# Kernel optimization log

Measured on AMD Instinct MI355X. Metric: run time of the kernel, lower is better.

## Reference

```python
import jax, jax.numpy as jnp
import numpy as np

S = 16          # spatial_size (adaptive pool output per dim)
EPS = 1e-8      # torch.cosine_similarity eps

def _avg_pool3d(x, s):
    # exact adaptive avg pool when D,H,W divisible by s
    B, C, D, H, W = x.shape
    kd, kh, kw = D // s, H // s, W // s
    x = x.reshape(B, C, s, kd, s, kh, s, kw)
    return x.mean(axis=(3, 5, 7))  # (B, C, s, s, s)

def _flatten_rows(x):
    # (B,C,s,s,s) -> (B*s^3, C), matching view+transpose+flatten
    B, C = x.shape[0], x.shape[1]
    return x.reshape(B, C, -1).transpose(0, 2, 1).reshape(-1, C)

def _cos_sim_matrix(a):
    # pairwise cosine similarity via normalize + GEMM
    norms = jnp.maximum(jnp.linalg.norm(a, axis=-1, keepdims=True), EPS)
    an = a / norms
    return an @ an.T  # (N, N)

def setup_inputs() -> dict:
    key = jax.random.key(0)
    k1, k2 = jax.random.split(key)
    shape = (2, 32, 64, 64, 64)
    p1 = jax.random.normal(k1, shape, dtype=jnp.float32)
    p2 = jax.random.normal(k2, shape, dtype=jnp.float32)
    return {"p1": p1, "p2": p2}

def reference(p1, p2):
    aa = _flatten_rows(_avg_pool3d(p1, S))  # (N, C), N = B*S^3
    bb = _flatten_rows(_avg_pool3d(p2, S))
    sim_a = _cos_sim_matrix(aa)
    sim_b = _cos_sim_matrix(bb)
    return jnp.mean((sim_a - sim_b) ** 2)  # MSELoss
```

## Files before the change

kernel.cpp:

```cpp
#include <hip/hip_runtime.h>
#include <hip/hip_bf16.h>


#define HW    4096
#define DHW   262144
#define NROW  8192
#define C     32
#define NPART 8

__global__ __launch_bounds__(1024) void pool_norm_kernel(
    const float* __restrict__ p1, const float* __restrict__ p2,
    float* __restrict__ An, float* __restrict__ Bn)
{
    const int bid = blockIdx.x;
    const int yo = bid & 15;
    const int zo = (bid >> 4) & 15;
    const int b  = bid >> 8;

    const float* __restrict__ src = (blockIdx.y == 0) ? p1 : p2;
    float* __restrict__ dst       = (blockIdx.y == 0) ? An : Bn;

    const int tid  = threadIdx.x;
    const int wv   = tid >> 6;
    const int lane = tid & 63;
    const int dy   = lane >> 4;
    const int x4   = lane & 15;

    __shared__ float pool[C][16];
    __shared__ float inv_norm[16];

    float4 v[2][4];
    #pragma unroll
    for (int cc = 0; cc < 2; ++cc) {
        const int c = wv * 2 + cc;
        const float* base = src + (size_t)(b * C + c) * DHW
                          + (4 * zo) * HW + (4 * yo + dy) * 64 + 4 * x4;
        #pragma unroll
        for (int dz = 0; dz < 4; ++dz)
            v[cc][dz] = *reinterpret_cast<const float4*>(base + dz * HW);
    }

    #pragma unroll
    for (int cc = 0; cc < 2; ++cc) {
        float s = 0.f;
        #pragma unroll
        for (int dz = 0; dz < 4; ++dz)
            s += (v[cc][dz].x + v[cc][dz].y) + (v[cc][dz].z + v[cc][dz].w);
        s += __shfl_xor(s, 16);
        s += __shfl_xor(s, 32);
        if (lane < 16) pool[wv * 2 + cc][lane] = s * (1.0f / 64.0f);
    }
    __syncthreads();

    if (tid < 16) {
        float ss = 0.f;
        #pragma unroll
        for (int c = 0; c < C; ++c) { const float p = pool[c][tid]; ss += p * p; }
        inv_norm[tid] = 1.0f / fmaxf(sqrtf(ss), 1e-8f);
    }
    __syncthreads();

    if (tid < 512) {
        const int x = tid >> 5;
        const int c = tid & 31;
        const int row = ((b * 16 + zo) * 16 + yo) * 16 + x;
        dst[(size_t)row * C + c] = pool[c][x] * inv_norm[x];
    }
}

__global__ __launch_bounds__(256) void gram_kernel(
    const float* __restrict__ An, const float* __restrict__ Bn,
    float* __restrict__ G)
{
    const int tid = threadIdx.x;
    const int k  = tid >> 3;
    const int l4 = (tid & 7) * 4;

    __shared__ float As[32 * C];
    __shared__ float Bs[32 * C];

    float gaa[4] = {0.f, 0.f, 0.f, 0.f};
    float gab[4] = {0.f, 0.f, 0.f, 0.f};
    float gbb[4] = {0.f, 0.f, 0.f, 0.f};

    const int r = blockIdx.x * 32;
    reinterpret_cast<float4*>(As)[tid] =
        reinterpret_cast<const float4*>(An + (size_t)r * C)[tid];
    reinterpret_cast<float4*>(Bs)[tid] =
        reinterpret_cast<const float4*>(Bn + (size_t)r * C)[tid];
    __syncthreads();

    #pragma unroll
    for (int i = 0; i < 32; ++i) {
        const float a_k = As[i * C + k];
        const float b_k = Bs[i * C + k];
        const float4 a_l = *reinterpret_cast<const float4*>(&As[i * C + l4]);
        const float4 b_l = *reinterpret_cast<const float4*>(&Bs[i * C + l4]);
        gaa[0] += a_k * a_l.x;  gaa[1] += a_k * a_l.y;
        gaa[2] += a_k * a_l.z;  gaa[3] += a_k * a_l.w;
        gab[0] += a_k * b_l.x;  gab[1] += a_k * b_l.y;
        gab[2] += a_k * b_l.z;  gab[3] += a_k * b_l.w;
        gbb[0] += b_k * b_l.x;  gbb[1] += b_k * b_l.y;
        gbb[2] += b_k * b_l.z;  gbb[3] += b_k * b_l.w;
    }

    float* Gp = G + (size_t)(blockIdx.x & (NPART - 1)) * 3072;
    #pragma unroll
    for (int j = 0; j < 4; ++j) {
        atomicAdd(&Gp[k * C + l4 + j],        gaa[j]);
        atomicAdd(&Gp[1024 + k * C + l4 + j], gab[j]);
        atomicAdd(&Gp[2048 + k * C + l4 + j], gbb[j]);
    }
}

__global__ __launch_bounds__(1024) void finalize_kernel(
    const float* __restrict__ G, float* __restrict__ out)
{
    const int t = threadIdx.x;
    float gaa = 0.f, gab = 0.f, gbb = 0.f;
    #pragma unroll
    for (int p = 0; p < NPART; ++p) {
        gaa += G[p * 3072 + t];
        gab += G[p * 3072 + 1024 + t];
        gbb += G[p * 3072 + 2048 + t];
    }
    float v = gaa * gaa + gbb * gbb - 2.f * gab * gab;

    __shared__ float red[16];
    #pragma unroll
    for (int off = 32; off > 0; off >>= 1) v += __shfl_down(v, off);
    if ((t & 63) == 0) red[t >> 6] = v;
    __syncthreads();
    if (t < 16) {
        float w = red[t];
        #pragma unroll
        for (int off = 8; off > 0; off >>= 1) w += __shfl_down(w, off);
        if (t == 0) out[0] = w / ((float)NROW * (float)NROW);
    }
}

extern "C" void kernel_launch(void* const* d_in, const int* in_sizes, int n_in,
                              void* d_out, int out_size, void* d_ws, size_t ws_size,
                              hipStream_t stream) {
    const float* p1 = (const float*)d_in[0];
    const float* p2 = (const float*)d_in[1];
    float* out = (float*)d_out;

    float* An = (float*)d_ws;
    float* Bn = An + (size_t)NROW * C;
    float* G  = Bn + (size_t)NROW * C;

    hipMemsetAsync(G, 0, NPART * 3072 * sizeof(float), stream);

    dim3 g1(512, 2);
    pool_norm_kernel<<<g1, 1024, 0, stream>>>(p1, p2, An, Bn);
    gram_kernel<<<256, 256, 0, stream>>>(An, Bn, G);
    finalize_kernel<<<1, 1024, 0, stream>>>(G, out);
}
```

Before: 160.7 us.

## Fuse pooling, normalization and Gram accumulation into one kernel

Merges the pool+normalize kernel and the Gram-matrix kernel into a single kernel. Each block loads both p1 and p2 tiles, pools and normalizes in shared memory, then computes its 32x32 partial Gram products directly and atomically adds them to 16 partition buffers. This removes the intermediate An/Bn round trip through global memory and one kernel launch. In exchange it halves the grid, doubles per-thread loads and registers, and raises atomic traffic, since 512 blocks now add 3072 values each.

```diff
diff --git a/kernel.cpp b/kernel.cpp
--- a/kernel.cpp
+++ b/kernel.cpp
@@ -6,19 +6,16 @@
 #define DHW   262144
 #define NROW  8192
 #define C     32
-#define NPART 8
+#define NPART 16
 
-__global__ __launch_bounds__(1024) void pool_norm_kernel(
+__global__ __launch_bounds__(1024) void fused_pool_gram_kernel(
     const float* __restrict__ p1, const float* __restrict__ p2,
-    float* __restrict__ An, float* __restrict__ Bn)
+    float* __restrict__ G)
 {
     const int bid = blockIdx.x;
     const int yo = bid & 15;
     const int zo = (bid >> 4) & 15;
     const int b  = bid >> 8;
-
-    const float* __restrict__ src = (blockIdx.y == 0) ? p1 : p2;
-    float* __restrict__ dst       = (blockIdx.y == 0) ? An : Bn;
 
     const int tid  = threadIdx.x;
     const int wv   = tid >> 6;
@@ -26,91 +23,86 @@
     const int dy   = lane >> 4;
     const int x4   = lane & 15;
 
-    __shared__ float pool[C][16];
-    __shared__ float inv_norm[16];
+    __shared__ float pa[C][17];
+    __shared__ float pb[C][17];
+    __shared__ float inva[16];
+    __shared__ float invb[16];
 
-    float4 v[2][4];
+    const size_t sp_off = (size_t)(4 * zo) * HW + (size_t)(4 * yo + dy) * 64 + 4 * x4;
+
+    float4 va[2][4], vb[2][4];
     #pragma unroll
     for (int cc = 0; cc < 2; ++cc) {
         const int c = wv * 2 + cc;
-        const float* base = src + (size_t)(b * C + c) * DHW
-                          + (4 * zo) * HW + (4 * yo + dy) * 64 + 4 * x4;
+        const float* basea = p1 + (size_t)(b * C + c) * DHW + sp_off;
+        const float* baseb = p2 + (size_t)(b * C + c) * DHW + sp_off;
         #pragma unroll
-        for (int dz = 0; dz < 4; ++dz)
-            v[cc][dz] = *reinterpret_cast<const float4*>(base + dz * HW);
+        for (int dz = 0; dz < 4; ++dz) {
+            va[cc][dz] = *reinterpret_cast<const float4*>(basea + dz * HW);
+            vb[cc][dz] = *reinterpret_cast<const float4*>(baseb + dz * HW);
+        }
     }
+    __builtin_amdgcn_sched_barrier(0);
 
     #pragma unroll
     for (int cc = 0; cc < 2; ++cc) {
-        float s = 0.f;
+        float sa = 0.f, sb = 0.f;
         #pragma unroll
-        for (int dz = 0; dz < 4; ++dz)
-            s += (v[cc][dz].x + v[cc][dz].y) + (v[cc][dz].z + v[cc][dz].w);
-        s += __shfl_xor(s, 16);
-        s += __shfl_xor(s, 32);
-        if (lane < 16) pool[wv * 2 + cc][lane] = s * (1.0f / 64.0f);
+        for (int dz = 0; dz < 4; ++dz) {
+            sa += (va[cc][dz].x + va[cc][dz].y) + (va[cc][dz].z + va[cc][dz].w);
+            sb += (vb[cc][dz].x + vb[cc][dz].y) + (vb[cc][dz].z + vb[cc][dz].w);
+        }
+        sa += __shfl_xor(sa, 16);  sa += __shfl_xor(sa, 32);
+        sb += __shfl_xor(sb, 16);  sb += __shfl_xor(sb, 32);
+        if (lane < 16) {
+            pa[wv * 2 + cc][lane] = sa * (1.0f / 64.0f);
+            pb[wv * 2 + cc][lane] = sb * (1.0f / 64.0f);
+        }
     }
     __syncthreads();
 
-    if (tid < 16) {
+    if (tid < 32) {
+        const int x = tid & 15;
         float ss = 0.f;
-        #pragma unroll
-        for (int c = 0; c < C; ++c) { const float p = pool[c][tid]; ss += p * p; }
-        inv_norm[tid] = 1.0f / fmaxf(sqrtf(ss), 1e-8f);
+        if (tid < 16) {
+            #pragma unroll
+            for (int c2 = 0; c2 < C; ++c2) { const float v = pa[c2][x]; ss += v * v; }
+            inva[x] = 1.0f / fmaxf(sqrtf(ss), 1e-8f);
+        } else {
+            #pragma unroll
+            for (int c2 = 0; c2 < C; ++c2) { const float v = pb[c2][x]; ss += v * v; }
+            invb[x] = 1.0f / fmaxf(sqrtf(ss), 1e-8f);
+        }
     }
     __syncthreads();
 
-    if (tid < 512) {
-        const int x = tid >> 5;
-        const int c = tid & 31;
-        const int row = ((b * 16 + zo) * 16 + yo) * 16 + x;
-        dst[(size_t)row * C + c] = pool[c][x] * inv_norm[x];
+    {
+        const int sel = tid >> 9;
+        const int c   = (tid >> 4) & 31;
+        const int x   = tid & 15;
+        if (sel == 0) pa[c][x] *= inva[x];
+        else          pb[c][x] *= invb[x];
     }
-}
-
-__global__ __launch_bounds__(256) void gram_kernel(
-    const float* __restrict__ An, const float* __restrict__ Bn,
-    float* __restrict__ G)
-{
-    const int tid = threadIdx.x;
-    const int k  = tid >> 3;
-    const int l4 = (tid & 7) * 4;
-
-    __shared__ float As[32 * C];
-    __shared__ float Bs[32 * C];
-
-    float gaa[4] = {0.f, 0.f, 0.f, 0.f};
-    float gab[4] = {0.f, 0.f, 0.f, 0.f};
-    float gbb[4] = {0.f, 0.f, 0.f, 0.f};
-
-    const int r = blockIdx.x * 32;
-    reinterpret_cast<float4*>(As)[tid] =
-        reinterpret_cast<const float4*>(An + (size_t)r * C)[tid];
-    reinterpret_cast<float4*>(Bs)[tid] =
-        reinterpret_cast<const float4*>(Bn + (size_t)r * C)[tid];
     __syncthreads();
 
+    const int k = tid >> 5;
+    const int l = tid & 31;
+    float gaa = 0.f, gab = 0.f, gbb = 0.f;
     #pragma unroll
-    for (int i = 0; i < 32; ++i) {
-        const float a_k = As[i * C + k];
-        const float b_k = Bs[i * C + k];
-        const float4 a_l = *reinterpret_cast<const float4*>(&As[i * C + l4]);
-        const float4 b_l = *reinterpret_cast<const float4*>(&Bs[i * C + l4]);
-        gaa[0] += a_k * a_l.x;  gaa[1] += a_k * a_l.y;
-        gaa[2] += a_k * a_l.z;  gaa[3] += a_k * a_l.w;
-        gab[0] += a_k * b_l.x;  gab[1] += a_k * b_l.y;
-        gab[2] += a_k * b_l.z;  gab[3] += a_k * b_l.w;
-        gbb[0] += b_k * b_l.x;  gbb[1] += b_k * b_l.y;
-        gbb[2] += b_k * b_l.z;  gbb[3] += b_k * b_l.w;
+    for (int x = 0; x < 16; ++x) {
+        const float ak = pa[k][x];
+        const float al = pa[l][x];
+        const float bk = pb[k][x];
+        const float bl = pb[l][x];
+        gaa += ak * al;
+        gab += ak * bl;
+        gbb += bk * bl;
     }
 
-    float* Gp = G + (size_t)(blockIdx.x & (NPART - 1)) * 3072;
-    #pragma unroll
-    for (int j = 0; j < 4; ++j) {
-        atomicAdd(&Gp[k * C + l4 + j],        gaa[j]);
-        atomicAdd(&Gp[1024 + k * C + l4 + j], gab[j]);
-        atomicAdd(&Gp[2048 + k * C + l4 + j], gbb[j]);
-    }
+    float* Gp = G + (size_t)(bid & (NPART - 1)) * 3072;
+    atomicAdd(&Gp[       k * 32 + l], gaa);
+    atomicAdd(&Gp[1024 + k * 32 + l], gab);
+    atomicAdd(&Gp[2048 + k * 32 + l], gbb);
 }
 
 __global__ __launch_bounds__(1024) void finalize_kernel(
@@ -146,14 +138,10 @@
     const float* p2 = (const float*)d_in[1];
     float* out = (float*)d_out;
 
-    float* An = (float*)d_ws;
-    float* Bn = An + (size_t)NROW * C;
-    float* G  = Bn + (size_t)NROW * C;
+    float* G = (float*)d_ws;
 
     hipMemsetAsync(G, 0, NPART * 3072 * sizeof(float), stream);
 
-    dim3 g1(512, 2);
-    pool_norm_kernel<<<g1, 1024, 0, stream>>>(p1, p2, An, Bn);
-    gram_kernel<<<256, 256, 0, stream>>>(An, Bn, G);
+    fused_pool_gram_kernel<<<512, 1024, 0, stream>>>(p1, p2, G);
     finalize_kernel<<<1, 1024, 0, stream>>>(G, out);
 }
```

Result: faster. 151.3 us (-5.8%).

## Restructure pooling for contiguous plane reads and fuse normalization into gram kernel

Applied to the files above, without the earlier changes.

The pooling kernel now gives each block one channel and a 16-plane slab. Each thread streams contiguous float4s across whole 64x64 planes, with 8 loads in flight per thread, instead of gathering scattered 4x4x4 tiles across channels. Row normalization moves out of pooling into the gram kernel, computed with wave shuffles on load, which removes the shared-memory reductions and syncs from pooling. The gram shared arrays are padded, and the number of atomic partial buffers is doubled to reduce contention. One cost is that pooled outputs are now written as strided scalar stores.

```diff
diff --git a/kernel.cpp b/kernel.cpp
--- a/kernel.cpp
+++ b/kernel.cpp
@@ -6,96 +6,97 @@
 #define DHW   262144
 #define NROW  8192
 #define C     32
-#define NPART 8
+#define NPART 16
 
-__global__ __launch_bounds__(1024) void pool_norm_kernel(
+__global__ __launch_bounds__(1024) void pool_kernel(
     const float* __restrict__ p1, const float* __restrict__ p2,
-    float* __restrict__ An, float* __restrict__ Bn)
+    float* __restrict__ A, float* __restrict__ B)
 {
-    const int bid = blockIdx.x;
-    const int yo = bid & 15;
-    const int zo = (bid >> 4) & 15;
-    const int b  = bid >> 8;
+    const int bid  = blockIdx.x;
+    const int slab = bid & 3;
+    const int c    = (bid >> 2) & 31;
+    const int b    = (bid >> 7) & 1;
+    const int sel  = bid >> 8;
 
-    const float* __restrict__ src = (blockIdx.y == 0) ? p1 : p2;
-    float* __restrict__ dst       = (blockIdx.y == 0) ? An : Bn;
+    const float* __restrict__ src = sel ? p2 : p1;
+    float* __restrict__ dst       = sel ? B : A;
 
     const int tid  = threadIdx.x;
     const int wv   = tid >> 6;
     const int lane = tid & 63;
-    const int dy   = lane >> 4;
-    const int x4   = lane & 15;
 
-    __shared__ float pool[C][16];
-    __shared__ float inv_norm[16];
-
-    float4 v[2][4];
-    #pragma unroll
-    for (int cc = 0; cc < 2; ++cc) {
-        const int c = wv * 2 + cc;
-        const float* base = src + (size_t)(b * C + c) * DHW
-                          + (4 * zo) * HW + (4 * yo + dy) * 64 + 4 * x4;
-        #pragma unroll
-        for (int dz = 0; dz < 4; ++dz)
-            v[cc][dz] = *reinterpret_cast<const float4*>(base + dz * HW);
-    }
+    const float* vol = src + (size_t)(b * C + c) * DHW + (size_t)(slab * 16) * HW;
 
     #pragma unroll
-    for (int cc = 0; cc < 2; ++cc) {
-        float s = 0.f;
+    for (int h = 0; h < 2; ++h) {
+        float4 v[8];
         #pragma unroll
-        for (int dz = 0; dz < 4; ++dz)
-            s += (v[cc][dz].x + v[cc][dz].y) + (v[cc][dz].z + v[cc][dz].w);
-        s += __shfl_xor(s, 16);
-        s += __shfl_xor(s, 32);
-        if (lane < 16) pool[wv * 2 + cc][lane] = s * (1.0f / 64.0f);
-    }
-    __syncthreads();
+        for (int rz = 0; rz < 8; ++rz)
+            v[rz] = *reinterpret_cast<const float4*>(
+                        vol + (size_t)(h * 8 + rz) * HW + (size_t)tid * 4);
+        __builtin_amdgcn_sched_barrier(0);
 
-    if (tid < 16) {
-        float ss = 0.f;
         #pragma unroll
-        for (int c = 0; c < C; ++c) { const float p = pool[c][tid]; ss += p * p; }
-        inv_norm[tid] = 1.0f / fmaxf(sqrtf(ss), 1e-8f);
-    }
-    __syncthreads();
-
-    if (tid < 512) {
-        const int x = tid >> 5;
-        const int c = tid & 31;
-        const int row = ((b * 16 + zo) * 16 + yo) * 16 + x;
-        dst[(size_t)row * C + c] = pool[c][x] * inv_norm[x];
+        for (int g = 0; g < 2; ++g) {
+            float s = 0.f;
+            #pragma unroll
+            for (int j = 0; j < 4; ++j) {
+                const float4 t = v[g * 4 + j];
+                s += (t.x + t.y) + (t.z + t.w);
+            }
+            s += __shfl_xor(s, 16);
+            s += __shfl_xor(s, 32);
+            if (lane < 16) {
+                const int zo  = slab * 4 + h * 2 + g;
+                const int row = ((b * 16 + zo) * 16 + wv) * 16 + lane;
+                dst[(size_t)row * C + c] = s * (1.0f / 64.0f);
+            }
+        }
     }
 }
 
 __global__ __launch_bounds__(256) void gram_kernel(
-    const float* __restrict__ An, const float* __restrict__ Bn,
+    const float* __restrict__ A, const float* __restrict__ B,
     float* __restrict__ G)
 {
     const int tid = threadIdx.x;
+    const int rl  = tid >> 3;
+    const int f4  = tid & 7;
+
+    __shared__ float As[32][36];
+    __shared__ float Bs[32][36];
+
+    const int r = blockIdx.x * 32 + rl;
+    float4 va = *reinterpret_cast<const float4*>(A + (size_t)r * C + f4 * 4);
+    float4 vb = *reinterpret_cast<const float4*>(B + (size_t)r * C + f4 * 4);
+
+    float ssa = va.x * va.x + va.y * va.y + va.z * va.z + va.w * va.w;
+    float ssb = vb.x * vb.x + vb.y * vb.y + vb.z * vb.z + vb.w * vb.w;
+    #pragma unroll
+    for (int off = 1; off < 8; off <<= 1) {
+        ssa += __shfl_xor(ssa, off);
+        ssb += __shfl_xor(ssb, off);
+    }
+    const float inva = 1.0f / fmaxf(sqrtf(ssa), 1e-8f);
+    const float invb = 1.0f / fmaxf(sqrtf(ssb), 1e-8f);
+    va.x *= inva; va.y *= inva; va.z *= inva; va.w *= inva;
+    vb.x *= invb; vb.y *= invb; vb.z *= invb; vb.w *= invb;
+    *reinterpret_cast<float4*>(&As[rl][f4 * 4]) = va;
+    *reinterpret_cast<float4*>(&Bs[rl][f4 * 4]) = vb;
+    __syncthreads();
+
     const int k  = tid >> 3;
     const int l4 = (tid & 7) * 4;
-
-    __shared__ float As[32 * C];
-    __shared__ float Bs[32 * C];
-
     float gaa[4] = {0.f, 0.f, 0.f, 0.f};
     float gab[4] = {0.f, 0.f, 0.f, 0.f};
     float gbb[4] = {0.f, 0.f, 0.f, 0.f};
 
-    const int r = blockIdx.x * 32;
-    reinterpret_cast<float4*>(As)[tid] =
-        reinterpret_cast<const float4*>(An + (size_t)r * C)[tid];
-    reinterpret_cast<float4*>(Bs)[tid] =
-        reinterpret_cast<const float4*>(Bn + (size_t)r * C)[tid];
-    __syncthreads();
-
     #pragma unroll
     for (int i = 0; i < 32; ++i) {
-        const float a_k = As[i * C + k];
-        const float b_k = Bs[i * C + k];
-        const float4 a_l = *reinterpret_cast<const float4*>(&As[i * C + l4]);
-        const float4 b_l = *reinterpret_cast<const float4*>(&Bs[i * C + l4]);
+        const float a_k = As[i][k];
+        const float b_k = Bs[i][k];
+        const float4 a_l = *reinterpret_cast<const float4*>(&As[i][l4]);
+        const float4 b_l = *reinterpret_cast<const float4*>(&Bs[i][l4]);
         gaa[0] += a_k * a_l.x;  gaa[1] += a_k * a_l.y;
         gaa[2] += a_k * a_l.z;  gaa[3] += a_k * a_l.w;
         gab[0] += a_k * b_l.x;  gab[1] += a_k * b_l.y;
@@ -107,7 +108,7 @@
     float* Gp = G + (size_t)(blockIdx.x & (NPART - 1)) * 3072;
     #pragma unroll
     for (int j = 0; j < 4; ++j) {
-        atomicAdd(&Gp[k * C + l4 + j],        gaa[j]);
+        atomicAdd(&Gp[       k * C + l4 + j], gaa[j]);
         atomicAdd(&Gp[1024 + k * C + l4 + j], gab[j]);
         atomicAdd(&Gp[2048 + k * C + l4 + j], gbb[j]);
     }
@@ -146,14 +147,13 @@
     const float* p2 = (const float*)d_in[1];
     float* out = (float*)d_out;
 
-    float* An = (float*)d_ws;
-    float* Bn = An + (size_t)NROW * C;
-    float* G  = Bn + (size_t)NROW * C;
+    float* A = (float*)d_ws;
+    float* B = A + (size_t)NROW * C;
+    float* G = B + (size_t)NROW * C;
 
     hipMemsetAsync(G, 0, NPART * 3072 * sizeof(float), stream);
 
-    dim3 g1(512, 2);
-    pool_norm_kernel<<<g1, 1024, 0, stream>>>(p1, p2, An, Bn);
-    gram_kernel<<<256, 256, 0, stream>>>(An, Bn, G);
+    pool_kernel<<<512, 1024, 0, stream>>>(p1, p2, A, B);
+    gram_kernel<<<256, 256, 0, stream>>>(A, B, G);
     finalize_kernel<<<1, 1024, 0, stream>>>(G, out);
 }
```

After: 162.0 us. About the same (+0.8%).
